# Kernel tuning notes

Measured on AMD Instinct MI355X. Metric: run time of the kernel, lower is better.

Reference implementation:

```python
import jax, jax.numpy as jnp
import numpy as np

C = 64
SIZE = 448
PATCH = 14
P2 = PATCH * PATCH                 # 196, per-chunk token count
SPLIT = (SIZE * SIZE) // P2        # 1024 chunks
TG = PATCH * 4                     # 56, pooled global resolution
POOL = SIZE // TG                  # 8, exact avg-pool factor
EPS = 1e-5


def setup_inputs() -> dict:
    key = jax.random.key(0)
    ks = jax.random.split(key, 10)
    b = 2
    x = jax.random.normal(ks[0], (b, C, SIZE, SIZE), dtype=jnp.float32)
    s = 1.0 / np.sqrt(C)
    return {
        "x": x,
        "gn_w": jnp.ones((C,), jnp.float32),
        "gn_b": jnp.zeros((C,), jnp.float32),
        "q_w": jax.random.normal(ks[1], (C, C), jnp.float32) * s,
        "q_b": jnp.zeros((C,), jnp.float32),
        "k_w": jax.random.normal(ks[2], (C, C), jnp.float32) * s,
        "k_b": jnp.zeros((C,), jnp.float32),
        "v_w": jax.random.normal(ks[3], (C, C), jnp.float32) * s,
        "v_b": jnp.zeros((C,), jnp.float32),
        "proj_w": jax.random.normal(ks[4], (C, C), jnp.float32) * s,
    }


def _conv1x1(t, W, bias=None):
    out = jnp.einsum('oc,bchw->bohw', W, t)
    if bias is not None:
        out = out + bias[None, :, None, None]
    return out


def _group_norm(x, w, b):
    # GroupNorm(num_groups=1): normalize over (C,H,W) per sample
    mean = x.mean(axis=(1, 2, 3), keepdims=True)
    var = x.var(axis=(1, 2, 3), keepdims=True)
    xn = (x - mean) * jax.lax.rsqrt(var + EPS)
    return xn * w[None, :, None, None] + b[None, :, None, None]


def reference(x, gn_w, gn_b, q_w, q_b, k_w, k_b, v_w, v_b, proj_w):
    b, c, h, w = x.shape
    xn = _group_norm(x, gn_w, gn_b)
    q = _conv1x1(xn, q_w, q_b)
    k = _conv1x1(xn, k_w, k_b)
    v = _conv1x1(xn, v_w, v_b)

    # ---- patch-local attention (channels*chunks as feature dim S) ----
    S = c * SPLIT  # 65536
    qf = q.reshape(b, S, P2)
    kf = k.reshape(b, S, P2)
    vf = v.reshape(b, S, P2)
    wm = jnp.einsum('bsp,bsq->bpq', qf, kf) * (S ** -0.5)  # [b,196,196]
    wm = jax.nn.softmax(wm, axis=2)
    # h[b,s,q'] = sum_k v[b,s,k] * wm[b,q',k]
    hp = jnp.einsum('bsk,bqk->bsq', vf, wm).reshape(b, c, h, w)

    # ---- global pooled attention ----
    pool = lambda t: t.reshape(b, c, TG, POOL, TG, POOL).mean(axis=(3, 5))
    qg = pool(q).reshape(b, c, TG * TG)
    kg = pool(k).reshape(b, c, TG * TG)
    vg = pool(v).reshape(b, c, TG * TG)
    wg = jnp.einsum('bcp,bcq->bpq', qg, kg) * (c ** -0.5)  # [b,3136,3136]
    wg = jax.nn.softmax(wg, axis=2)
    hg = jnp.einsum('bck,bqk->bcq', vg, wg).reshape(b, c, TG, TG)
    hg = jnp.repeat(jnp.repeat(hg, POOL, axis=2), POOL, axis=3)

    h_in = 0.75 * hp + 0.25 * hg
    out = _conv1x1(h_in, proj_w)  # proj_out, no bias
    return x + out
```

## Files before the change

kernel.cpp:

```cpp
#include <hip/hip_runtime.h>

#define NB 2
#define NC 64
#define HW 200704
#define CHW 12845056
#define P2 196
#define NCHUNK 1024
#define NCELL 3136
#define WMN 38416

typedef __attribute__((ext_vector_type(8))) short bfrag;
typedef __attribute__((ext_vector_type(4))) float ffrag;
typedef __attribute__((ext_vector_type(4))) short short4v;
typedef __attribute__((ext_vector_type(4))) float float4v;

#define MFMA16(A,B,C) __builtin_amdgcn_mfma_f32_16x16x32_bf16(A,B,C,0,0,0)

__device__ __forceinline__ short f2bf(float f) {
  unsigned u = __builtin_bit_cast(unsigned, f);
  u = u + 0x7FFFu + ((u >> 16) & 1u);
  return (short)(u >> 16);
}

__global__ __launch_bounds__(256) void k0_fold(
    const float* __restrict__ pw, const float* __restrict__ vw,
    const float* __restrict__ vb, float* __restrict__ wtld, float* __restrict__ btld) {
  int t = threadIdx.x;
  if (blockIdx.x == 0) {
    #pragma unroll
    for (int i = 0; i < 16; ++i) {
      int idx = i*256 + t;
      int o = idx >> 6, c = idx & 63;
      float s = 0.f;
      for (int m = 0; m < 64; ++m) s += pw[o*64 + m] * vw[m*64 + c];
      wtld[o*64 + c] = s;
    }
  } else {
    if (t < 64) {
      float s = 0.f;
      for (int m = 0; m < 64; ++m) s += pw[t*64 + m] * vb[m];
      btld[t] = s;
    }
  }
}

__global__ __launch_bounds__(64) void k1_stats_pool(
    const float* __restrict__ x, float* __restrict__ xpool, float* __restrict__ partials) {
  int bx = blockIdx.x;
  int batch = bx / (64*56);
  int c = (bx / 56) % 64;
  int pr = bx % 56;
  int l = threadIdx.x;
  const float* xp = x + (size_t)batch*CHW + (size_t)c*HW + pr*8*448;
  float cell = 0.f, s2 = 0.f;
  if (l < 56) {
    #pragma unroll
    for (int r = 0; r < 8; ++r) {
      float4v a = *(const float4v*)(xp + r*448 + l*8);
      float4v b = *(const float4v*)(xp + r*448 + l*8 + 4);
      #pragma unroll
      for (int j = 0; j < 4; ++j) { cell += a[j] + b[j]; s2 += a[j]*a[j] + b[j]*b[j]; }
    }
    xpool[((size_t)batch*64 + c)*NCELL + pr*56 + l] = cell * (1.f/64.f);
  }
  float s1 = (l < 56) ? cell : 0.f;
  #pragma unroll
  for (int m = 1; m < 64; m <<= 1) { s1 += __shfl_xor(s1, m, 64); s2 += __shfl_xor(s2, m, 64); }
  if (l == 0) { partials[bx*2] = s1; partials[bx*2 + 1] = s2; }
}

__global__ __launch_bounds__(256) void k1b_reduce(
    const float* __restrict__ partials, float* __restrict__ stats) {
  __shared__ float red[2][256];
  int t = threadIdx.x;
  for (int b = 0; b < NB; ++b) {
    float s1 = 0.f, s2 = 0.f;
    for (int i = t; i < 3584; i += 256) {
      s1 += partials[(b*3584 + i)*2];
      s2 += partials[(b*3584 + i)*2 + 1];
    }
    red[0][t] = s1; red[1][t] = s2;
    __syncthreads();
    for (int m = 128; m > 0; m >>= 1) {
      if (t < m) { red[0][t] += red[0][t+m]; red[1][t] += red[1][t+m]; }
      __syncthreads();
    }
    if (t == 0) { stats[b*2] = red[0][0]; stats[b*2+1] = red[1][0]; }
    __syncthreads();
  }
}

__global__ __launch_bounds__(256) void k0b_foldgn(
    const float* __restrict__ stats, const float* __restrict__ gnw, const float* __restrict__ gnb,
    const float* __restrict__ qw, const float* __restrict__ qb,
    const float* __restrict__ kw, const float* __restrict__ kb,
    const float* __restrict__ vw, const float* __restrict__ vb,
    short* __restrict__ qwb, short* __restrict__ kwb, short* __restrict__ vwb,
    float* __restrict__ qbb, float* __restrict__ kbb, float* __restrict__ vbb) {
  __shared__ float a_s[64], d_s[64];
  int batch = blockIdx.x;
  int t = threadIdx.x;
  float s1 = stats[batch*2], s2 = stats[batch*2+1];
  float mean = s1 * (1.f/CHW);
  float rstd = rsqrtf(s2*(1.f/CHW) - mean*mean + 1e-5f);
  if (t < 64) { float a = rstd*gnw[t]; a_s[t] = a; d_s[t] = gnb[t] - mean*a; }
  __syncthreads();
  const float* Ws[3] = {qw, kw, vw};
  const float* Bs[3] = {qb, kb, vb};
  short* Wo[3] = {qwb, kwb, vwb};
  float* Bo[3] = {qbb, kbb, vbb};
  for (int T = 0; T < 3; ++T) {
    #pragma unroll
    for (int i = 0; i < 16; ++i) {
      int idx = i*256 + t;
      int c = idx & 63;
      Wo[T][batch*4096 + idx] = f2bf(Ws[T][idx] * a_s[c]);
    }
    if (t < 64) {
      float s = Bs[T][t];
      for (int c = 0; c < 64; ++c) s += Ws[T][t*64 + c] * d_s[c];
      Bo[T][batch*64 + t] = s;
    }
  }
}

__global__ __launch_bounds__(256) void k2_qkv(
    const float* __restrict__ x,
    const short* __restrict__ qwb, const short* __restrict__ kwb, const short* __restrict__ vwb,
    const float* __restrict__ qbb, const float* __restrict__ kbb, const float* __restrict__ vbb,
    short* __restrict__ qx, short* __restrict__ kx, short* __restrict__ vnat) {
  __shared__ __attribute__((aligned(16))) short xnt[256*72];
  int bx = blockIdx.x;
  int batch = bx / 784;
  int px0 = (bx % 784) * 256;
  int t = threadIdx.x;
  for (int it = 0; it < 64; it += 4) {
    short4v s;
    #pragma unroll
    for (int r = 0; r < 4; ++r)
      s[r] = f2bf(x[(size_t)batch*CHW + (size_t)(it+r)*HW + px0 + t]);
    *(short4v*)(xnt + t*72 + it) = s;
  }
  __syncthreads();
  int l = t & 63, w = t >> 6, li = l & 15, q_ = l >> 4;
  bfrag bfr[4][2];
  #pragma unroll
  for (int nn = 0; nn < 4; ++nn) {
    int row = (w*4 + nn)*16 + li;
    bfr[nn][0] = *(const bfrag*)(xnt + row*72 + q_*8);
    bfr[nn][1] = *(const bfrag*)(xnt + row*72 + 32 + q_*8);
  }
  const short* Wb[3] = {qwb + batch*4096, kwb + batch*4096, vwb + batch*4096};
  const float* Bb[3] = {qbb + batch*64, kbb + batch*64, vbb + batch*64};
  for (int T = 0; T < 3; ++T) {
    ffrag acc[4][4];
    #pragma unroll
    for (int mt = 0; mt < 4; ++mt) {
      bfrag aw0 = *(const bfrag*)(Wb[T] + (mt*16 + li)*64 + q_*8);
      bfrag aw1 = *(const bfrag*)(Wb[T] + (mt*16 + li)*64 + 32 + q_*8);
      #pragma unroll
      for (int nn = 0; nn < 4; ++nn) {
        ffrag z = {0.f,0.f,0.f,0.f};
        if (T < 2) {
          z = MFMA16(aw0, bfr[nn][0], z);
          z = MFMA16(aw1, bfr[nn][1], z);
        } else {
          z = MFMA16(bfr[nn][0], aw0, z);
          z = MFMA16(bfr[nn][1], aw1, z);
        }
        acc[mt][nn] = z;
      }
    }
    if (T < 2) {
      short* dstb = (T == 0 ? qx : kx) + (size_t)batch*HW*64;
      #pragma unroll
      for (int nn = 0; nn < 4; ++nn) {
        int px = px0 + (w*4 + nn)*16 + li;
        #pragma unroll
        for (int mt = 0; mt < 4; ++mt) {
          float4v bias = *(const float4v*)(Bb[T] + mt*16 + q_*4);
          short4v s;
          #pragma unroll
          for (int r = 0; r < 4; ++r) s[r] = f2bf(acc[mt][nn][r] + bias[r]);
          *(short4v*)(dstb + (size_t)px*64 + mt*16 + q_*4) = s;
        }
      }
    } else {
      #pragma unroll
      for (int mt = 0; mt < 4; ++mt) {
        float bias = Bb[2][mt*16 + li];
        short* vrow = vnat + ((size_t)batch*64 + mt*16 + li)*HW + px0;
        #pragma unroll
        for (int nn = 0; nn < 4; ++nn) {
          short4v s;
          #pragma unroll
          for (int r = 0; r < 4; ++r) s[r] = f2bf(acc[mt][nn][r] + bias);
          *(short4v*)(vrow + (w*4 + nn)*16 + q_*4) = s;
        }
      }
    }
  }
}

__global__ __launch_bounds__(256) void k2a_pool_qkv(
    const float* __restrict__ xpool, const float* __restrict__ stats,
    const float* __restrict__ gnw, const float* __restrict__ gnb,
    const float* __restrict__ qw, const float* __restrict__ qb,
    const float* __restrict__ kw, const float* __restrict__ kb,
    const float* __restrict__ vw, const float* __restrict__ vb,
    short* __restrict__ qgt, short* __restrict__ kgt, short* __restrict__ vgn) {
  __shared__ float xs[64][64];
  int bx = blockIdx.x;
  int batch = bx / 49;
  int j0 = (bx % 49) * 64;
  int t = threadIdx.x;
  float s1 = stats[batch*2], s2 = stats[batch*2+1];
  float mean = s1 * (1.f/CHW);
  float rstd = rsqrtf(s2*(1.f/CHW) - mean*mean + 1e-5f);
  #pragma unroll
  for (int it = 0; it < 16; ++it) {
    int idx = t + it*256;
    int c = idx >> 6, jl = idx & 63;
    float v = xpool[((size_t)batch*64 + c)*NCELL + j0 + jl];
    xs[c][jl] = (v - mean)*rstd*gnw[c] + gnb[c];
  }
  __syncthreads();
  int jl = t & 63;
  int og = (t >> 6) * 16;
  int j = j0 + jl;
  for (int T = 0; T < 3; ++T) {
    const float* W  = (T==0 ? qw : (T==1 ? kw : vw));
    const float* Bv = (T==0 ? qb : (T==1 ? kb : vb));
    float o16[16];
    #pragma unroll
    for (int oo = 0; oo < 16; ++oo) o16[oo] = Bv[og+oo];
    for (int c = 0; c < 64; ++c) {
      float xv = xs[c][jl];
      #pragma unroll
      for (int oo = 0; oo < 16; ++oo) o16[oo] += W[(og+oo)*64 + c] * xv;
    }
    if (T < 2) {
      short* dst = (T==0 ? qgt : kgt) + ((size_t)batch*NCELL + j)*64 + og;
      #pragma unroll
      for (int oo = 0; oo < 16; oo += 4) {
        short4v s;
        #pragma unroll
        for (int r = 0; r < 4; ++r) s[r] = f2bf(o16[oo+r]);
        *(short4v*)(dst + oo) = s;
      }
    } else {
      #pragma unroll
      for (int oo = 0; oo < 16; ++oo)
        vgn[((size_t)batch*64 + og + oo)*NCELL + j] = f2bf(o16[oo]);
    }
  }
}

__global__ __launch_bounds__(256) void k3_wm(
    const short* __restrict__ qx, const short* __restrict__ kx, float* __restrict__ wmacc) {
  int bx = blockIdx.x;
  int batch = bx >> 8;
  int rem = bx & 255;
  int slab = rem >> 2;
  int qd = rem & 3;
  int t = threadIdx.x;
  int l = t & 63, w = t >> 6, li = l & 15, q_ = l >> 4;
  int m0 = w ? 4 + (w-1)*3 : 0, mcnt = w ? 3 : 4;
  int nt0 = qd ? 4 + (qd-1)*3 : 0, ncnt = qd ? 3 : 4;
  ffrag acc[4][4];
  #pragma unroll
  for (int i = 0; i < 4; ++i)
    #pragma unroll
    for (int j = 0; j < 4; ++j) acc[i][j] = (ffrag){0.f,0.f,0.f,0.f};
  const short* qbase = qx + (size_t)batch*HW*64;
  const short* kbase = kx + (size_t)batch*HW*64;
  for (int c8 = 0; c8 < 16; ++c8) {
    int chunk = slab*16 + c8;
    const short* qc = qbase + (size_t)chunk*P2*64;
    const short* kc = kbase + (size_t)chunk*P2*64;
    #pragma unroll
    for (int ks = 0; ks < 2; ++ks) {
      int koff = ks*32 + q_*8;
      bfrag af[4], bf[4];
      #pragma unroll
      for (int mi = 0; mi < 4; ++mi) if (mi < mcnt)
        af[mi] = *(const bfrag*)(qc + (size_t)((m0+mi)*16 + li)*64 + koff);
      #pragma unroll
      for (int ni = 0; ni < 4; ++ni) if (ni < ncnt)
        bf[ni] = *(const bfrag*)(kc + (size_t)((nt0+ni)*16 + li)*64 + koff);
      #pragma unroll
      for (int mi = 0; mi < 4; ++mi) if (mi < mcnt)
        #pragma unroll
        for (int ni = 0; ni < 4; ++ni) if (ni < ncnt)
          acc[mi][ni] = MFMA16(af[mi], bf[ni], acc[mi][ni]);
    }
  }
  float* wdst = wmacc + (size_t)batch*WMN;
  #pragma unroll
  for (int mi = 0; mi < 4; ++mi) if (mi < mcnt)
    #pragma unroll
    for (int ni = 0; ni < 4; ++ni) if (ni < ncnt) {
      int qcol = (nt0+ni)*16 + li;
      if (qcol < 196)
        #pragma unroll
        for (int r = 0; r < 4; ++r) {
          int prow = (m0+mi)*16 + q_*4 + r;
          if (prow < 196) atomicAdd(wdst + prow*196 + qcol, acc[mi][ni][r]);
        }
    }
}

__global__ __launch_bounds__(64) void k4_softmax(
    const float* __restrict__ wmacc, short* __restrict__ P) {
  int bx = blockIdx.x;
  int batch = bx / 208;
  int p = bx % 208;
  int l = threadIdx.x;
  short* prow = P + ((size_t)batch*208 + p)*224;
  if (p >= 196) { for (int j = l; j < 224; j += 64) prow[j] = 0; return; }
  const float* src = wmacc + (size_t)batch*WMN + p*196;
  float v[4]; float mx = -1e30f;
  #pragma unroll
  for (int i = 0; i < 4; ++i) {
    int q = l + i*64;
    v[i] = (q < 196) ? src[q]*(1.f/256.f) : -1e30f;
    mx = fmaxf(mx, v[i]);
  }
  #pragma unroll
  for (int m = 1; m < 64; m <<= 1) mx = fmaxf(mx, __shfl_xor(mx, m, 64));
  float s = 0.f;
  #pragma unroll
  for (int i = 0; i < 4; ++i) { v[i] = __expf(v[i] - mx); s += v[i]; }
  #pragma unroll
  for (int m = 1; m < 64; m <<= 1) s += __shfl_xor(s, m, 64);
  float inv = 0.75f / s;
  #pragma unroll
  for (int i = 0; i < 4; ++i) {
    int q = l + i*64;
    if (q < 224) prow[q] = (q < 196) ? f2bf(v[i]*inv) : (short)0;
  }
}

__global__ __launch_bounds__(256) void k5_gattn(
    const short* __restrict__ qgt, const short* __restrict__ kgt,
    const short* __restrict__ vgn, float* __restrict__ hgt) {
  __shared__ __attribute__((aligned(16))) short Pl[4][16][72];
  __shared__ __attribute__((aligned(16))) float alph[4][16];
  __shared__ __attribute__((aligned(16))) float Om[4][16][64];
  __shared__ __attribute__((aligned(16))) float ml[4][2][16];
  int bx = blockIdx.x;
  int batch = bx / 196;
  int i0 = (bx % 196) * 16;
  int t = threadIdx.x;
  int w = t >> 6, l = t & 63, li = l & 15, q_ = l >> 4;
  const short* qg = qgt + (size_t)batch*NCELL*64;
  const short* kg = kgt + (size_t)batch*NCELL*64;
  const short* vg = vgn + (size_t)batch*64*NCELL;
  bfrag bq0 = *(const bfrag*)(qg + (size_t)(i0+li)*64 + q_*8);
  bfrag bq1 = *(const bfrag*)(qg + (size_t)(i0+li)*64 + 32 + q_*8);
  float m_run = -1e30f, l_run = 0.f;
  ffrag oa[4];
  #pragma unroll
  for (int i = 0; i < 4; ++i) oa[i] = (ffrag){0.f,0.f,0.f,0.f};
  for (int jt = w; jt < 49; jt += 4) {
    int j0 = jt*64;
    ffrag st[4];
    #pragma unroll
    for (int mt = 0; mt < 4; ++mt) {
      bfrag a0 = *(const bfrag*)(kg + (size_t)(j0 + mt*16 + li)*64 + q_*8);
      bfrag a1 = *(const bfrag*)(kg + (size_t)(j0 + mt*16 + li)*64 + 32 + q_*8);
      ffrag z = {0.f,0.f,0.f,0.f};
      z = MFMA16(a0, bq0, z);
      z = MFMA16(a1, bq1, z);
      st[mt] = z;
    }
    float mx = -1e30f;
    #pragma unroll
    for (int mt = 0; mt < 4; ++mt)
      #pragma unroll
      for (int r = 0; r < 4; ++r) { st[mt][r] *= 0.125f; mx = fmaxf(mx, st[mt][r]); }
    mx = fmaxf(mx, __shfl_xor(mx, 16, 64));
    mx = fmaxf(mx, __shfl_xor(mx, 32, 64));
    float m_new = fmaxf(m_run, mx);
    float alpha = __expf(m_run - m_new);
    float ps = 0.f;
    short4v pk[4];
    #pragma unroll
    for (int mt = 0; mt < 4; ++mt)
      #pragma unroll
      for (int r = 0; r < 4; ++r) { float e = __expf(st[mt][r] - m_new); ps += e; pk[mt][r] = f2bf(e); }
    ps += __shfl_xor(ps, 16, 64);
    ps += __shfl_xor(ps, 32, 64);
    l_run = l_run*alpha + ps;
    m_run = m_new;
    #pragma unroll
    for (int mt = 0; mt < 4; ++mt) *(short4v*)(&Pl[w][li][mt*16 + q_*4]) = pk[mt];
    alph[w][li] = alpha;
    float4v al = *(const float4v*)(&alph[w][q_*4]);
    #pragma unroll
    for (int nt = 0; nt < 4; ++nt)
      #pragma unroll
      for (int r = 0; r < 4; ++r) oa[nt][r] *= al[r];
    #pragma unroll
    for (int ks = 0; ks < 2; ++ks) {
      bfrag a = *(const bfrag*)(&Pl[w][li][ks*32 + q_*8]);
      #pragma unroll
      for (int nt = 0; nt < 4; ++nt) {
        bfrag b = *(const bfrag*)(vg + (size_t)(nt*16 + li)*NCELL + j0 + ks*32 + q_*8);
        oa[nt] = MFMA16(a, b, oa[nt]);
      }
    }
  }
  ml[w][0][li] = m_run;
  ml[w][1][li] = l_run;
  #pragma unroll
  for (int nt = 0; nt < 4; ++nt)
    #pragma unroll
    for (int r = 0; r < 4; ++r)
      Om[w][q_*4 + r][nt*16 + li] = oa[nt][r];
  __syncthreads();
  int qq = t >> 4, c4 = (t & 15) * 4;
  float m0 = ml[0][0][qq], m1 = ml[1][0][qq], m2 = ml[2][0][qq], m3 = ml[3][0][qq];
  float ms = fmaxf(fmaxf(m0, m1), fmaxf(m2, m3));
  float s0 = __expf(m0 - ms), s1 = __expf(m1 - ms);
  float s2 = __expf(m2 - ms), s3 = __expf(m3 - ms);
  float lt = ml[0][1][qq]*s0 + ml[1][1][qq]*s1 + ml[2][1][qq]*s2 + ml[3][1][qq]*s3;
  float inv = 1.f / lt;
  float sw[4] = {s0, s1, s2, s3};
  float4v o = {0.f, 0.f, 0.f, 0.f};
  #pragma unroll
  for (int w2 = 0; w2 < 4; ++w2) {
    float4v ov = *(const float4v*)(&Om[w2][qq][c4]);
    #pragma unroll
    for (int r = 0; r < 4; ++r) o[r] += ov[r] * sw[w2];
  }
  float4v outv;
  #pragma unroll
  for (int r = 0; r < 4; ++r) outv[r] = o[r] * inv;
  *(float4v*)(hgt + (size_t)batch*NCELL*64 + (size_t)(i0 + qq)*64 + c4) = outv;
}

__global__ __launch_bounds__(256) void k6_hp_out(
    const short* __restrict__ vtld, const short* __restrict__ P,
    const float* __restrict__ hgt,
    const float* __restrict__ x, float* __restrict__ out) {
  __shared__ __attribute__((aligned(16))) short smem[64*232];
  short* vch = smem;
  short* fsb = smem;
  int bx = blockIdx.x;
  int batch = bx >> 10;
  int chunk = bx & 1023;
  int t = threadIdx.x;
  const short* vsrc = vtld + (size_t)batch*64*HW + chunk*P2;
  for (int idx = t; idx < 3136; idx += 256) {
    int c = idx / 49, po = idx % 49;
    *(short4v*)(vch + c*232 + po*4) = *(const short4v*)(vsrc + (size_t)c*HW + po*4);
  }
  for (int idx = t; idx < 448; idx += 256) {
    int c = idx / 7, po = idx % 7;
    *(short4v*)(vch + c*232 + 196 + po*4) = (short4v){0,0,0,0};
  }
  __syncthreads();
  int l = t & 63, w = t >> 6, li = l & 15, q_ = l >> 4;
  int nt0 = w ? 4 + (w-1)*3 : 0;
  int ncnt = w ? 3 : 4;
  const short* Pb = P + (size_t)batch*208*224;
  ffrag acc[4][4];
  #pragma unroll
  for (int i = 0; i < 4; ++i)
    #pragma unroll
    for (int j = 0; j < 4; ++j) acc[i][j] = (ffrag){0.f,0.f,0.f,0.f};
  #pragma unroll
  for (int ks = 0; ks < 7; ++ks) {
    int koff = ks*32 + q_*8;
    bfrag av[4];
    #pragma unroll
    for (int mt = 0; mt < 4; ++mt) av[mt] = *(const bfrag*)(vch + (mt*16 + li)*232 + koff);
    #pragma unroll
    for (int ni = 0; ni < 4; ++ni) if (ni < ncnt) {
      bfrag bp = *(const bfrag*)(Pb + (size_t)((nt0+ni)*16 + li)*224 + koff);
      #pragma unroll
      for (int mt = 0; mt < 4; ++mt) acc[mt][ni] = MFMA16(av[mt], bp, acc[mt][ni]);
    }
  }
  __syncthreads();
  #pragma unroll
  for (int ni = 0; ni < 4; ++ni) if (ni < ncnt) {
    int pp = (nt0+ni)*16 + li;
    if (pp < 196) {
      #pragma unroll
      for (int mt = 0; mt < 4; ++mt)
        #pragma unroll
        for (int r = 0; r < 4; ++r)
          fsb[(mt*16 + q_*4 + r)*204 + pp] = f2bf(acc[mt][ni][r]);
    }
  }
  __syncthreads();
  const float* hgb = hgt + (size_t)batch*NCELL*64;
  const float* xb = x + (size_t)batch*CHW;
  float* ob = out + (size_t)batch*CHW;
  int gbase = chunk*P2;
  for (int idx = t; idx < 3136; idx += 256) {
    int c = idx / 49, po = idx % 49;
    int g = gbase + po*4;
    int cell = ((g/448) >> 3)*56 + ((g%448) >> 3);
    float hr = 0.25f * hgb[cell*64 + c];
    size_t off = (size_t)c*HW + (size_t)gbase + po*4;
    float4v xv = *(const float4v*)(xb + off);
    short4v fb = *(const short4v*)(fsb + c*204 + po*4);
    float4v o;
    #pragma unroll
    for (int r = 0; r < 4; ++r) {
      float fv = __builtin_bit_cast(float, ((unsigned)(unsigned short)fb[r]) << 16);
      o[r] = xv[r] + fv + hr;
    }
    *(float4v*)(ob + off) = o;
  }
}

extern "C" void kernel_launch(void* const* d_in, const int* in_sizes, int n_in,
                              void* d_out, int out_size, void* d_ws, size_t ws_size,
                              hipStream_t stream) {
  (void)in_sizes; (void)n_in; (void)out_size; (void)ws_size;
  const float* x   = (const float*)d_in[0];
  const float* gnw = (const float*)d_in[1];
  const float* gnb = (const float*)d_in[2];
  const float* qw  = (const float*)d_in[3];
  const float* qb  = (const float*)d_in[4];
  const float* kw  = (const float*)d_in[5];
  const float* kb  = (const float*)d_in[6];
  const float* vw  = (const float*)d_in[7];
  const float* vb  = (const float*)d_in[8];
  const float* pw  = (const float*)d_in[9];
  float* out = (float*)d_out;
  char* ws = (char*)d_ws;

  short* qx    = (short*)(ws + 0);
  short* kx    = (short*)(ws + 51380224);
  short* vnat  = (short*)(ws + 102760448);
  float* xpool = (float*)(ws + 154140672);
  short* qgt   = (short*)(ws + 155746304);
  short* kgt   = (short*)(ws + 156549120);
  short* vgn   = (short*)(ws + 157351936);
  float* hgt   = (float*)(ws + 158154752);
  short* P     = (short*)(ws + 159760384);
  float* wmacc = (float*)(ws + 159946752);
  float* stats = (float*)(ws + 160254080);
  float* partials = (float*)(ws + 159760384);
  float* wtld = (float*)(ws + 158154752);
  float* btld = (float*)(ws + 158154752 + 16384);
  short* qwb  = (short*)(ws + 158154752 + 32768);
  short* kwb  = (short*)(ws + 158154752 + 49152);
  short* vwb  = (short*)(ws + 158154752 + 65536);
  float* qbb  = (float*)(ws + 158154752 + 81920);
  float* kbb  = (float*)(ws + 158154752 + 82432);
  float* vbb  = (float*)(ws + 158154752 + 82944);

  hipMemsetAsync(ws + 159946752, 0, 307328, stream);
  k0_fold      <<<dim3(2),        dim3(256), 0, stream>>>(pw, vw, vb, wtld, btld);
  k1_stats_pool<<<dim3(NB*64*56), dim3(64),  0, stream>>>(x, xpool, partials);
  k1b_reduce   <<<dim3(1),        dim3(256), 0, stream>>>(partials, stats);
  k0b_foldgn   <<<dim3(NB),       dim3(256), 0, stream>>>(stats, gnw, gnb, qw, qb, kw, kb, wtld, btld, qwb, kwb, vwb, qbb, kbb, vbb);
  k2_qkv       <<<dim3(NB*784),   dim3(256), 0, stream>>>(x, qwb, kwb, vwb, qbb, kbb, vbb, qx, kx, vnat);
  k2a_pool_qkv <<<dim3(NB*49),    dim3(256), 0, stream>>>(xpool, stats, gnw, gnb, qw, qb, kw, kb, wtld, btld, qgt, kgt, vgn);
  k3_wm        <<<dim3(NB*256),   dim3(256), 0, stream>>>(qx, kx, wmacc);
  k4_softmax   <<<dim3(NB*208),   dim3(64),  0, stream>>>(wmacc, P);
  k5_gattn     <<<dim3(NB*196),   dim3(256), 0, stream>>>(qgt, kgt, vgn, hgt);
  k6_hp_out    <<<dim3(NB*1024),  dim3(256), 0, stream>>>(vnat, P, hgt, x, out);
}
```

Baseline: 577.4 us.

## Split k3_wm row tiles across twice the blocks and double-buffer fragment loads

```diff
diff --git a/kernel.cpp b/kernel.cpp
--- a/kernel.cpp
+++ b/kernel.cpp
@@ -259,45 +259,54 @@
 __global__ __launch_bounds__(256) void k3_wm(
     const short* __restrict__ qx, const short* __restrict__ kx, float* __restrict__ wmacc) {
   int bx = blockIdx.x;
-  int batch = bx >> 8;
-  int rem = bx & 255;
-  int slab = rem >> 2;
+  int batch = bx >> 9;
+  int rem = bx & 511;
+  int slab = rem >> 3;
+  int mh = (rem >> 2) & 1;
   int qd = rem & 3;
   int t = threadIdx.x;
   int l = t & 63, w = t >> 6, li = l & 15, q_ = l >> 4;
-  int m0 = w ? 4 + (w-1)*3 : 0, mcnt = w ? 3 : 4;
+  int m0, mcnt;
+  if (mh == 0) { m0 = w*2;                    mcnt = (w < 3) ? 2 : 1; }
+  else         { m0 = (w < 2) ? 7 + w*2 : 9 + w; mcnt = (w < 2) ? 2 : 1; }
   int nt0 = qd ? 4 + (qd-1)*3 : 0, ncnt = qd ? 3 : 4;
-  ffrag acc[4][4];
-  #pragma unroll
-  for (int i = 0; i < 4; ++i)
+  ffrag acc[2][4];
+  #pragma unroll
+  for (int i = 0; i < 2; ++i)
     #pragma unroll
     for (int j = 0; j < 4; ++j) acc[i][j] = (ffrag){0.f,0.f,0.f,0.f};
-  const short* qbase = qx + (size_t)batch*HW*64;
-  const short* kbase = kx + (size_t)batch*HW*64;
-  for (int c8 = 0; c8 < 16; ++c8) {
-    int chunk = slab*16 + c8;
-    const short* qc = qbase + (size_t)chunk*P2*64;
-    const short* kc = kbase + (size_t)chunk*P2*64;
-    #pragma unroll
-    for (int ks = 0; ks < 2; ++ks) {
-      int koff = ks*32 + q_*8;
-      bfrag af[4], bf[4];
-      #pragma unroll
-      for (int mi = 0; mi < 4; ++mi) if (mi < mcnt)
-        af[mi] = *(const bfrag*)(qc + (size_t)((m0+mi)*16 + li)*64 + koff);
+  const short* qbase = qx + ((size_t)batch*HW + (size_t)slab*16*P2)*64;
+  const short* kbase = kx + ((size_t)batch*HW + (size_t)slab*16*P2)*64;
+  bfrag afA[2], bfA[4], afB[2], bfB[4];
+  auto ld = [&](int s, bfrag* af, bfrag* bf) {
+    int c8 = s >> 1;
+    int koff = (s & 1)*32 + q_*8;
+    const short* qc = qbase + (size_t)c8*P2*64;
+    const short* kc = kbase + (size_t)c8*P2*64;
+    #pragma unroll
+    for (int mi = 0; mi < 2; ++mi) if (mi < mcnt)
+      af[mi] = *(const bfrag*)(qc + (size_t)((m0+mi)*16 + li)*64 + koff);
+    #pragma unroll
+    for (int ni = 0; ni < 4; ++ni) if (ni < ncnt)
+      bf[ni] = *(const bfrag*)(kc + (size_t)((nt0+ni)*16 + li)*64 + koff);
+  };
+  auto mm = [&](bfrag* af, bfrag* bf) {
+    #pragma unroll
+    for (int mi = 0; mi < 2; ++mi) if (mi < mcnt)
       #pragma unroll
       for (int ni = 0; ni < 4; ++ni) if (ni < ncnt)
-        bf[ni] = *(const bfrag*)(kc + (size_t)((nt0+ni)*16 + li)*64 + koff);
-      #pragma unroll
-      for (int mi = 0; mi < 4; ++mi) if (mi < mcnt)
-        #pragma unroll
-        for (int ni = 0; ni < 4; ++ni) if (ni < ncnt)
-          acc[mi][ni] = MFMA16(af[mi], bf[ni], acc[mi][ni]);
-    }
+        acc[mi][ni] = MFMA16(af[mi], bf[ni], acc[mi][ni]);
+  };
+  ld(0, afA, bfA);
+  for (int s = 0; s < 32; s += 2) {
+    ld(s+1, afB, bfB);
+    mm(afA, bfA);
+    if (s+2 < 32) ld(s+2, afA, bfA);
+    mm(afB, bfB);
   }
   float* wdst = wmacc + (size_t)batch*WMN;
   #pragma unroll
-  for (int mi = 0; mi < 4; ++mi) if (mi < mcnt)
+  for (int mi = 0; mi < 2; ++mi) if (mi < mcnt)
     #pragma unroll
     for (int ni = 0; ni < 4; ++ni) if (ni < ncnt) {
       int qcol = (nt0+ni)*16 + li;
@@ -563,7 +572,7 @@
   k0b_foldgn   <<<dim3(NB),       dim3(256), 0, stream>>>(stats, gnw, gnb, qw, qb, kw, kb, wtld, btld, qwb, kwb, vwb, qbb, kbb, vbb);
   k2_qkv       <<<dim3(NB*784),   dim3(256), 0, stream>>>(x, qwb, kwb, vwb, qbb, kbb, vbb, qx, kx, vnat);
   k2a_pool_qkv <<<dim3(NB*49),    dim3(256), 0, stream>>>(xpool, stats, gnw, gnb, qw, qb, kw, kb, wtld, btld, qgt, kgt, vgn);
-  k3_wm        <<<dim3(NB*256),   dim3(256), 0, stream>>>(qx, kx, wmacc);
+  k3_wm        <<<dim3(NB*512),   dim3(256), 0, stream>>>(qx, kx, wmacc);
   k4_softmax   <<<dim3(NB*208),   dim3(64),  0, stream>>>(wmacc, P);
   k5_gattn     <<<dim3(NB*196),   dim3(256), 0, stream>>>(qgt, kgt, vgn, hgt);
   k6_hp_out    <<<dim3(NB*1024),  dim3(256), 0, stream>>>(vnat, P, hgt, x, out);
```

Result: no change. 579.7 us (+0.4%).
